# Performance work log

Hardware: AMD Instinct MI355X
Metric: run time of the kernel (lower is better)

The kernel has to match this reference:

```python
import jax, jax.numpy as jnp
import numpy as np

H = 8        # heads
W = 64       # window size
SHIFT = True
DIM = 512
SCALE = (DIM // H) ** -0.5


def setup_inputs() -> dict:
    key = jax.random.key(0)
    k1, k2, k3, k4 = jax.random.split(key, 4)
    x = jax.random.normal(k1, (8, 4096, DIM), dtype=jnp.float32)
    w_qkv = jax.random.normal(k2, (3 * DIM, DIM), dtype=jnp.float32) * 0.02
    w_proj = jax.random.normal(k3, (DIM, DIM), dtype=jnp.float32) * 0.02
    b_proj = jax.random.normal(k4, (DIM,), dtype=jnp.float32) * 0.02
    return {"x": x, "w_qkv": w_qkv, "w_proj": w_proj, "b_proj": b_proj}


def reference(x, w_qkv, w_proj, b_proj):
    B, N, C = x.shape
    if SHIFT:
        x = jnp.roll(x, -W // 2, axis=1)
    pad = (W - N % W) % W  # static Python int
    if pad:
        x = jnp.pad(x, ((0, 0), (0, pad), (0, 0)))
    nw = x.shape[1] // W
    xw = x.reshape(B * nw, W, C)                     # (B', W, C)
    qkv = xw @ w_qkv.T                               # (B', W, 3C)
    qkv = qkv.reshape(B * nw, W, 3, H, C // H)
    q, k, v = qkv[:, :, 0], qkv[:, :, 1], qkv[:, :, 2]  # (B', W, H, dh)
    # NOTE: faithful to source -- heads are NOT moved before matmul, so
    # attention is over the head axis: attn shape (B', W, H, H).
    attn = jnp.einsum('bwhd,bwgd->bwhg', q, k) * SCALE
    attn = jax.nn.softmax(attn, axis=-1)
    out = jnp.einsum('bwhg,bwgd->bwhd', attn, v)     # (B', W, H, dh)
    # transpose(1,2) then raw reshape, exactly as torch does (channel scramble)
    out = out.transpose(0, 2, 1, 3).reshape(B * nw, W, C)
    out = out @ w_proj.T + b_proj
    out = out.reshape(B, nw * W, C)[:, :N]
    if SHIFT:
        out = jnp.roll(out, W // 2, axis=1)
    return out
```

## Files before the change

### kernel.cpp

```cpp
#include <hip/hip_runtime.h>
#include <math.h>

typedef __attribute__((ext_vector_type(8))) short short8;
typedef __attribute__((ext_vector_type(4))) float float4v;

#define KDIM  512
#define NQKV  1536

__device__ __forceinline__ unsigned short f2bf(float f) {
    unsigned int u = __float_as_uint(f);
    u += 0x7FFFu + ((u >> 16) & 1u);
    return (unsigned short)(u >> 16);
}
__device__ __forceinline__ float bf2f(unsigned short u) {
    return __uint_as_float(((unsigned int)u) << 16);
}

__device__ __forceinline__ void gl2lds16(const unsigned short* g, unsigned short* l) {
    __builtin_amdgcn_global_load_lds(
        (const __attribute__((address_space(1))) void*)g,
        (__attribute__((address_space(3))) void*)l, 16, 0, 0);
}

__global__ __launch_bounds__(256) void cast_x_kernel(const float* __restrict__ x,
                                                     unsigned short* __restrict__ xb) {
    int tid = blockIdx.x * 256 + threadIdx.x;
    int t = tid >> 7;
    int c = (tid & 127) << 2;
    int b = t >> 12, n = t & 4095;
    int src = (b << 12) | ((n + 32) & 4095);
    float4 v = *(const float4*)(x + (((size_t)src) << 9) + c);
    ushort4 o;
    o.x = f2bf(v.x); o.y = f2bf(v.y); o.z = f2bf(v.z); o.w = f2bf(v.w);
    *(ushort4*)(xb + (((size_t)t) << 9) + c) = o;
}

__global__ __launch_bounds__(256) void cast_w_kernel(const float* __restrict__ wqkv,
                                                     const float* __restrict__ wproj,
                                                     unsigned short* __restrict__ wqkvb,
                                                     unsigned short* __restrict__ wprojb) {
    int tid = blockIdx.x * 256 + threadIdx.x;
    int e = tid << 2;
    if (e < NQKV * KDIM) {
        float4 v = *(const float4*)(wqkv + e);
        ushort4 o; o.x = f2bf(v.x); o.y = f2bf(v.y); o.z = f2bf(v.z); o.w = f2bf(v.w);
        *(ushort4*)(wqkvb + e) = o;
    } else {
        int e2 = e - NQKV * KDIM;
        float4 v = *(const float4*)(wproj + e2);
        ushort4 o; o.x = f2bf(v.x); o.y = f2bf(v.y); o.z = f2bf(v.z); o.w = f2bf(v.w);
        *(ushort4*)(wprojb + e2) = o;
    }
}

template<int N, bool PROJ>
__global__ __launch_bounds__(256, 2) void gemm_kernel(
        const unsigned short* __restrict__ A,
        const unsigned short* __restrict__ B,
        unsigned short* __restrict__ Cb,
        float* __restrict__ Cf,
        const float* __restrict__ bias) {
    __shared__ __align__(16) unsigned short As[128 * 32];
    __shared__ __align__(16) unsigned short Bs[128 * 32];
    const int bn = blockIdx.x, bm = blockIdx.y;
    const int tid = threadIdx.x;
    const int wave = tid >> 6, lane = tid & 63;
    const int quad = lane >> 4, l16 = lane & 15;
    const int wm = (wave >> 1) * 64, wn = (wave & 1) * 64;
    const int srow = lane >> 2;
    const int scol = (lane & 3) * 8;

    float4v acc[4][4] = {};

    const unsigned short* Abase = A + (size_t)(bm * 128) * KDIM;
    const unsigned short* Bbase = B + (size_t)(bn * 128) * KDIM;

    for (int k0 = 0; k0 < KDIM; k0 += 32) {
        #pragma unroll
        for (int j = 0; j < 2; j++) {
            int chunk = j * 4 + wave;
            int row = chunk * 16 + srow;
            gl2lds16(Abase + (size_t)row * KDIM + k0 + scol, As + chunk * 512);
            gl2lds16(Bbase + (size_t)row * KDIM + k0 + scol, Bs + chunk * 512);
        }
        __syncthreads();
        short8 af[4], bf[4];
        #pragma unroll
        for (int mi = 0; mi < 4; mi++)
            af[mi] = *(const short8*)(As + (wm + mi * 16 + l16) * 32 + quad * 8);
        #pragma unroll
        for (int ni = 0; ni < 4; ni++)
            bf[ni] = *(const short8*)(Bs + (wn + ni * 16 + l16) * 32 + quad * 8);
        #pragma unroll
        for (int mi = 0; mi < 4; mi++)
            #pragma unroll
            for (int ni = 0; ni < 4; ni++)
                acc[mi][ni] = __builtin_amdgcn_mfma_f32_16x16x32_bf16(
                    af[mi], bf[ni], acc[mi][ni], 0, 0, 0);
        __syncthreads();
    }

    #pragma unroll
    for (int mi = 0; mi < 4; mi++) {
        #pragma unroll
        for (int r = 0; r < 4; r++) {
            int m = bm * 128 + wm + mi * 16 + quad * 4 + r;
            if (!PROJ) {
                #pragma unroll
                for (int ni = 0; ni < 4; ni++) {
                    int n = bn * 128 + wn + ni * 16 + l16;
                    Cb[(size_t)m * N + n] = f2bf(acc[mi][ni][r]);
                }
            } else {
                int b = m >> 12, p = m & 4095;
                int nrow = (p + 32) & 4095;
                float* orow = Cf + (((size_t)((b << 12) | nrow)) << 9);
                #pragma unroll
                for (int ni = 0; ni < 4; ni++) {
                    int n = bn * 128 + wn + ni * 16 + l16;
                    orow[n] = acc[mi][ni][r] + bias[n];
                }
            }
        }
    }
}

#define TPB_TOK 16
#define LDS_STRIDE 1544
__global__ __launch_bounds__(128) void attn_kernel(const unsigned short* __restrict__ qkvb,
                                                   unsigned short* __restrict__ aob) {
    __shared__ __align__(16) unsigned short smem[TPB_TOK * LDS_STRIDE];
    const int tid = threadIdx.x;
    const int t0 = blockIdx.x * TPB_TOK;

    {
        int r = tid >> 3, cb = (tid & 7) * 8;
        const unsigned short* src = qkvb + (size_t)(t0 + r) * NQKV;
        unsigned short* dst = smem + r * LDS_STRIDE;
        #pragma unroll
        for (int p = 0; p < 24; p++) {
            int c = cb + p * 64;
            *(short8*)(dst + c) = *(const short8*)(src + c);
        }
    }
    __syncthreads();

    const int tok = tid >> 3, h = tid & 7;
    const unsigned short* row = smem + tok * LDS_STRIDE;

    float qv[64];
    #pragma unroll
    for (int dc = 0; dc < 8; dc++) {
        short8 qs = *(const short8*)(row + h * 64 + dc * 8);
        #pragma unroll
        for (int j = 0; j < 8; j++)
            qv[dc * 8 + j] = bf2f((unsigned short)qs[j]);
    }

    float s[8];
    #pragma unroll
    for (int g = 0; g < 8; g++) {
        float acc = 0.f;
        #pragma unroll
        for (int dc = 0; dc < 8; dc++) {
            short8 ks = *(const short8*)(row + 512 + g * 64 + dc * 8);
            #pragma unroll
            for (int j = 0; j < 8; j++)
                acc += qv[dc * 8 + j] * bf2f((unsigned short)ks[j]);
        }
        s[g] = acc;
    }

    float mx = s[0];
    #pragma unroll
    for (int g = 1; g < 8; g++) mx = fmaxf(mx, s[g]);
    float p[8], sum = 0.f;
    #pragma unroll
    for (int g = 0; g < 8; g++) { p[g] = __expf((s[g] - mx) * 0.125f); sum += p[g]; }
    float inv = 1.f / sum;
    #pragma unroll
    for (int g = 0; g < 8; g++) p[g] *= inv;

    float o[64];
    #pragma unroll
    for (int j = 0; j < 64; j++) o[j] = 0.f;
    #pragma unroll
    for (int g = 0; g < 8; g++) {
        #pragma unroll
        for (int dc = 0; dc < 8; dc++) {
            short8 vs = *(const short8*)(row + 1024 + g * 64 + dc * 8);
            #pragma unroll
            for (int j = 0; j < 8; j++)
                o[dc * 8 + j] += p[g] * bf2f((unsigned short)vs[j]);
        }
    }

    int t = t0 + tok, win = t >> 6, w = t & 63;
    unsigned short* dst = aob + (size_t)(win * 64 + h * 8 + (w >> 3)) * 512 + (w & 7) * 64;
    #pragma unroll
    for (int dc = 0; dc < 16; dc++) {
        ushort4 ov;
        ov.x = f2bf(o[dc * 4 + 0]); ov.y = f2bf(o[dc * 4 + 1]);
        ov.z = f2bf(o[dc * 4 + 2]); ov.w = f2bf(o[dc * 4 + 3]);
        *(ushort4*)(dst + dc * 4) = ov;
    }
}

extern "C" void kernel_launch(void* const* d_in, const int* in_sizes, int n_in,
                              void* d_out, int out_size, void* d_ws, size_t ws_size,
                              hipStream_t stream) {
    const float* x      = (const float*)d_in[0];
    const float* w_qkv  = (const float*)d_in[1];
    const float* w_proj = (const float*)d_in[2];
    const float* b_proj = (const float*)d_in[3];
    float* out = (float*)d_out;

    char* ws = (char*)d_ws;
    unsigned short* xb     = (unsigned short*)(ws);
    unsigned short* wqkvb  = (unsigned short*)(ws + 33554432);
    unsigned short* wprojb = (unsigned short*)(ws + 35127296);
    unsigned short* qkvb   = (unsigned short*)(ws + 35651584);
    unsigned short* aob    = (unsigned short*)(ws + 136314880);

    cast_x_kernel<<<16384, 256, 0, stream>>>(x, xb);
    cast_w_kernel<<<1024, 256, 0, stream>>>(w_qkv, w_proj, wqkvb, wprojb);
    gemm_kernel<NQKV, false><<<dim3(12, 256), 256, 0, stream>>>(xb, wqkvb, qkvb, nullptr, nullptr);
    attn_kernel<<<2048, 128, 0, stream>>>(qkvb, aob);
    gemm_kernel<512, true><<<dim3(4, 256), 256, 0, stream>>>(aob, wprojb, nullptr, out, b_proj);
}
```

Measured before the change: 257.6 us.

## Double GEMM K-tile to 64 with XOR-swizzled LDS and direct Q loads in attention

The GEMM now stages 64-wide K slices per iteration, so there are half as many barrier pairs. The LDS layout uses an XOR swizzle on 16-byte blocks to avoid bank conflicts on the MFMA fragment reads. The attention kernel loads each thread's Q slice straight from global memory into registers and stages only K and V in LDS, which cuts LDS footprint and copy traffic. The larger GEMM tiles double LDS use per block, which may affect occupancy.

```diff
diff --git a/kernel.cpp b/kernel.cpp
--- a/kernel.cpp
+++ b/kernel.cpp
@@ -60,43 +60,52 @@
         unsigned short* __restrict__ Cb,
         float* __restrict__ Cf,
         const float* __restrict__ bias) {
-    __shared__ __align__(16) unsigned short As[128 * 32];
-    __shared__ __align__(16) unsigned short Bs[128 * 32];
+    __shared__ __align__(16) unsigned short As[128 * 64];
+    __shared__ __align__(16) unsigned short Bs[128 * 64];
     const int bn = blockIdx.x, bm = blockIdx.y;
     const int tid = threadIdx.x;
     const int wave = tid >> 6, lane = tid & 63;
     const int quad = lane >> 4, l16 = lane & 15;
     const int wm = (wave >> 1) * 64, wn = (wave & 1) * 64;
-    const int srow = lane >> 2;
-    const int scol = (lane & 3) * 8;
+    const int srow = lane >> 3;
+    const int scol = ((lane & 7) ^ srow) * 8;
 
     float4v acc[4][4] = {};
 
     const unsigned short* Abase = A + (size_t)(bm * 128) * KDIM;
     const unsigned short* Bbase = B + (size_t)(bn * 128) * KDIM;
 
-    for (int k0 = 0; k0 < KDIM; k0 += 32) {
-        #pragma unroll
-        for (int j = 0; j < 2; j++) {
+    for (int k0 = 0; k0 < KDIM; k0 += 64) {
+        #pragma unroll
+        for (int j = 0; j < 4; j++) {
             int chunk = j * 4 + wave;
-            int row = chunk * 16 + srow;
+            int row = chunk * 8 + srow;
             gl2lds16(Abase + (size_t)row * KDIM + k0 + scol, As + chunk * 512);
             gl2lds16(Bbase + (size_t)row * KDIM + k0 + scol, Bs + chunk * 512);
         }
         __syncthreads();
-        short8 af[4], bf[4];
-        #pragma unroll
-        for (int mi = 0; mi < 4; mi++)
-            af[mi] = *(const short8*)(As + (wm + mi * 16 + l16) * 32 + quad * 8);
-        #pragma unroll
-        for (int ni = 0; ni < 4; ni++)
-            bf[ni] = *(const short8*)(Bs + (wn + ni * 16 + l16) * 32 + quad * 8);
-        #pragma unroll
-        for (int mi = 0; mi < 4; mi++)
-            #pragma unroll
-            for (int ni = 0; ni < 4; ni++)
-                acc[mi][ni] = __builtin_amdgcn_mfma_f32_16x16x32_bf16(
-                    af[mi], bf[ni], acc[mi][ni], 0, 0, 0);
+        #pragma unroll
+        for (int ki = 0; ki < 2; ki++) {
+            short8 af[4], bf[4];
+            #pragma unroll
+            for (int mi = 0; mi < 4; mi++) {
+                int r = wm + mi * 16 + l16;
+                int blk = (ki * 4 + quad) ^ (l16 & 7);
+                af[mi] = *(const short8*)(As + r * 64 + blk * 8);
+            }
+            #pragma unroll
+            for (int ni = 0; ni < 4; ni++) {
+                int r = wn + ni * 16 + l16;
+                int blk = (ki * 4 + quad) ^ (l16 & 7);
+                bf[ni] = *(const short8*)(Bs + r * 64 + blk * 8);
+            }
+            #pragma unroll
+            for (int mi = 0; mi < 4; mi++)
+                #pragma unroll
+                for (int ni = 0; ni < 4; ni++)
+                    acc[mi][ni] = __builtin_amdgcn_mfma_f32_16x16x32_bf16(
+                        af[mi], bf[ni], acc[mi][ni], 0, 0, 0);
+        }
         __syncthreads();
     }
 
@@ -126,36 +135,43 @@
 }
 
 #define TPB_TOK 16
-#define LDS_STRIDE 1544
+#define KV_STRIDE 1032
 __global__ __launch_bounds__(128) void attn_kernel(const unsigned short* __restrict__ qkvb,
                                                    unsigned short* __restrict__ aob) {
-    __shared__ __align__(16) unsigned short smem[TPB_TOK * LDS_STRIDE];
+    __shared__ __align__(16) unsigned short smem[TPB_TOK * KV_STRIDE];
     const int tid = threadIdx.x;
     const int t0 = blockIdx.x * TPB_TOK;
+    const int tok = tid >> 3, h = tid & 7;
+    const int t = t0 + tok;
+
+    short8 qs[8];
+    {
+        const unsigned short* qsrc = qkvb + (size_t)t * NQKV + h * 64;
+        #pragma unroll
+        for (int dc = 0; dc < 8; dc++)
+            qs[dc] = *(const short8*)(qsrc + dc * 8);
+    }
 
     {
         int r = tid >> 3, cb = (tid & 7) * 8;
-        const unsigned short* src = qkvb + (size_t)(t0 + r) * NQKV;
-        unsigned short* dst = smem + r * LDS_STRIDE;
-        #pragma unroll
-        for (int p = 0; p < 24; p++) {
+        const unsigned short* src = qkvb + (size_t)(t0 + r) * NQKV + 512;
+        unsigned short* dst = smem + r * KV_STRIDE;
+        #pragma unroll
+        for (int p = 0; p < 16; p++) {
             int c = cb + p * 64;
             *(short8*)(dst + c) = *(const short8*)(src + c);
         }
     }
     __syncthreads();
 
-    const int tok = tid >> 3, h = tid & 7;
-    const unsigned short* row = smem + tok * LDS_STRIDE;
+    const unsigned short* row = smem + tok * KV_STRIDE;
 
     float qv[64];
     #pragma unroll
-    for (int dc = 0; dc < 8; dc++) {
-        short8 qs = *(const short8*)(row + h * 64 + dc * 8);
+    for (int dc = 0; dc < 8; dc++)
         #pragma unroll
         for (int j = 0; j < 8; j++)
-            qv[dc * 8 + j] = bf2f((unsigned short)qs[j]);
-    }
+            qv[dc * 8 + j] = bf2f((unsigned short)qs[dc][j]);
 
     float s[8];
     #pragma unroll
@@ -163,7 +179,7 @@
         float acc = 0.f;
         #pragma unroll
         for (int dc = 0; dc < 8; dc++) {
-            short8 ks = *(const short8*)(row + 512 + g * 64 + dc * 8);
+            short8 ks = *(const short8*)(row + g * 64 + dc * 8);
             #pragma unroll
             for (int j = 0; j < 8; j++)
                 acc += qv[dc * 8 + j] * bf2f((unsigned short)ks[j]);
@@ -188,14 +204,14 @@
     for (int g = 0; g < 8; g++) {
         #pragma unroll
         for (int dc = 0; dc < 8; dc++) {
-            short8 vs = *(const short8*)(row + 1024 + g * 64 + dc * 8);
+            short8 vs = *(const short8*)(row + 512 + g * 64 + dc * 8);
             #pragma unroll
             for (int j = 0; j < 8; j++)
                 o[dc * 8 + j] += p[g] * bf2f((unsigned short)vs[j]);
         }
     }
 
-    int t = t0 + tok, win = t >> 6, w = t & 63;
+    int win = t >> 6, w = t & 63;
     unsigned short* dst = aob + (size_t)(win * 64 + h * 8 + (w >> 3)) * 512 + (w & 7) * 64;
     #pragma unroll
     for (int dc = 0; dc < 16; dc++) {
```

After: 251.5 us. 1.02x faster.
